# Kernel tuning notes

Hardware: AMD Instinct MI355X
Metric: run time of the kernel (lower is better)

The kernel has to match this reference:

```python
import jax, jax.numpy as jnp
import numpy as np

B, N, C = 4, 4096, 1024
H, D = 16, 64
EPS = 1e-6


def setup_inputs() -> dict:
    key = jax.random.key(0)
    ks = jax.random.split(key, 7)
    x = jax.random.normal(ks[0], (B, N, C), dtype=jnp.float32)
    # True = PAD (PyTorch convention)
    src_key_padding_mask = jax.random.randint(ks[1], (B, N), 0, 2).astype(jnp.bool_)
    s = 1.0 / np.sqrt(C)
    W_qkv = jax.random.uniform(ks[2], (3 * C, C), jnp.float32, -s, s)
    b_qkv = jax.random.uniform(ks[3], (3 * C,), jnp.float32, -s, s)
    W_out = jax.random.uniform(ks[4], (C, C), jnp.float32, -s, s)
    b_out = jax.random.uniform(ks[5], (C,), jnp.float32, -s, s)
    return {"x": x, "W_qkv": W_qkv, "b_qkv": b_qkv, "W_out": W_out,
            "b_out": b_out, "src_key_padding_mask": src_key_padding_mask}


def _phi(t):
    # elu(t) + 1  (alpha=1)
    return jnp.where(t > 0, t + 1.0, jnp.exp(t))


def reference(x, W_qkv, b_qkv, W_out, b_out, src_key_padding_mask):
    # qkv projection: [B,N,3C] -> [3,B,H,N,D]
    qkv = (x @ W_qkv.T + b_qkv).reshape(B, N, 3, H, D).transpose(2, 0, 3, 1, 4)
    q, k, v = qkv[0], qkv[1], qkv[2]
    qf = _phi(q)
    kf = _phi(k)
    valid = (~src_key_padding_mask).astype(kf.dtype)[:, None, :, None]  # [B,1,N,1]
    kf = kf * valid
    v = v * valid
    # kv state: [B,H,D,D]; z: [B,H,D]
    kv = jnp.einsum('bhnd,bhne->bhde', kf, v)
    z = kf.sum(axis=2)
    y_num = jnp.einsum('bhnd,bhde->bhne', qf, kv)      # [B,H,N,D]
    y_den = jnp.einsum('bhnd,bhd->bhn', qf, z)          # [B,H,N]
    y_den = jnp.maximum(y_den, EPS)[..., None]
    y = (y_num / y_den).transpose(0, 2, 1, 3).reshape(B, N, C)
    return y @ W_out.T + b_out
```

## Files before the change

kernel.cpp:

```cpp
#include <hip/hip_runtime.h>
#include <math.h>

#define B_ 4
#define N_ 4096
#define C_ 1024
#define H_ 16
#define D_ 64
#define M_ (B_*N_)
#define GK 1024
#define NCH 8
#define CHROWS (N_/NCH)

typedef __attribute__((ext_vector_type(8))) _Float16 f16x8;
typedef __attribute__((ext_vector_type(4))) _Float16 f16x4;
typedef __attribute__((ext_vector_type(4))) float f32x4;

__device__ __forceinline__ float phi_f(float t) {
  return (t > 0.0f) ? (t + 1.0f) : __expf(t);
}

#define GLOAD(gp, lp) __builtin_amdgcn_global_load_lds( \
    (const __attribute__((address_space(1))) unsigned int*)(gp), \
    (__attribute__((address_space(3))) unsigned int*)(lp), 16, 0, 0)

#define BARM() asm volatile("s_barrier" ::: "memory")
#define WAITV6() asm volatile("s_waitcnt vmcnt(6)" ::: "memory")
#define WAITV4() asm volatile("s_waitcnt vmcnt(4)" ::: "memory")
#define WAITV0() asm volatile("s_waitcnt vmcnt(0)" ::: "memory")
#define PRIO1() __builtin_amdgcn_s_setprio(1)
#define PRIO0() __builtin_amdgcn_s_setprio(0)

__device__ __forceinline__ f32x4 mfma16h(f16x8 a, f16x8 b, f32x4 c) {
  return __builtin_amdgcn_mfma_f32_16x16x32_f16(a, b, c, 0, 0, 0);
}

__global__ __launch_bounds__(256) void mask_detect_k(const unsigned int* __restrict__ w,
                                                     int* __restrict__ flag) {
  __shared__ int notint, notflt;
  if (threadIdx.x == 0) { notint = 0; notflt = 0; }
  __syncthreads();
  int ni = 0, nf = 0;
  for (int i = threadIdx.x; i < 4096; i += 256) {
    unsigned int v = w[i];
    if (v > 1u) ni = 1;
    if (v != 0u && v != 0x3F800000u) nf = 1;
  }
  if (ni) atomicOr(&notint, 1);
  if (nf) atomicOr(&notflt, 1);
  __syncthreads();
  if (threadIdx.x == 0) *flag = (!notint) ? 0 : ((!notflt) ? 1 : 2);
}

__global__ __launch_bounds__(256) void mask_convert_k(const void* __restrict__ mask,
                                                      const int* __restrict__ flag,
                                                      float* __restrict__ valid) {
  int i = blockIdx.x * 256 + threadIdx.x;
  int f = *flag;
  int m;
  if (f == 0)      m = ((const int*)mask)[i] != 0;
  else if (f == 1) m = ((const float*)mask)[i] != 0.0f;
  else             m = ((const unsigned char*)mask)[i] != 0;
  valid[i] = m ? 0.0f : 1.0f;
}

__global__ __launch_bounds__(256) void conv_f16_k(const float* __restrict__ src,
                                                  _Float16* __restrict__ dst, int n4) {
  int i = blockIdx.x * 256 + threadIdx.x;
  if (i >= n4) return;
  float4 v = ((const float4*)src)[i];
  f16x4 h;
  h[0] = (_Float16)v.x; h[1] = (_Float16)v.y;
  h[2] = (_Float16)v.z; h[3] = (_Float16)v.w;
  ((f16x4*)dst)[i] = h;
}

__global__ __launch_bounds__(256) void split_f16_k(const float* __restrict__ src,
                                                   _Float16* __restrict__ h,
                                                   _Float16* __restrict__ l, int n4) {
  int i = blockIdx.x * 256 + threadIdx.x;
  if (i >= n4) return;
  float4 v = ((const float4*)src)[i];
  f16x4 hv, lv;
  float vs[4] = {v.x, v.y, v.z, v.w};
#pragma unroll
  for (int q = 0; q < 4; ++q) {
    _Float16 hh = (_Float16)vs[q];
    _Float16 ll = (_Float16)(vs[q] - (float)hh);
    hv[q] = hh; lv[q] = ll;
  }
  ((f16x4*)h)[i] = hv;
  ((f16x4*)l)[i] = lv;
}


#define TILE_BODY(PC, DO_STAGE, DO_PRE, WAITK, KS)                             \
  {                                                                            \
    const _Float16* bb = lds + (PC) * 24576;                                   \
    const _Float16* nb = lds + (((PC) + 1) % 3) * 24576;                       \
    _Float16* sq = lds + (((PC) + 2) % 3) * 24576;                             \
    const size_t ks = (KS);                                                    \
                                     \
    _Pragma("unroll") for (int j = 0; j < 4; ++j)                              \
      bl[j] = *(const f16x8*)&bb[16384 + (wj * 4 + j) * 512 + lane * 8];       \
    if (DO_STAGE) { GLOAD(A + gA0 + ks, sq + w * 512);                         \
                    GLOAD(A + gA1 + ks, sq + 4096 + w * 512); }                \
    BARM();                                                                    \
    PRIO1();                                                                   \
    _Pragma("unroll") for (int i = 0; i < 4; ++i)                              \
      _Pragma("unroll") for (int j = 0; j < 4; ++j)                            \
        acc[i][j] = mfma16h(a0[i], bh[j], acc[i][j]);                          \
    PRIO0();                                                                   \
        \
    _Pragma("unroll") for (int i = 0; i < 4; ++i)                              \
      a1[i] = *(const f16x8*)&bb[(wm * 8 + 4 + i) * 512 + lane * 8];           \
    if (DO_STAGE) { GLOAD(Bh + gB0 + ks, sq + 8192 + w * 512);                 \
                    GLOAD(Bh + gB1 + ks, sq + 12288 + w * 512); }              \
    if ((WAITK) == 1) { WAITV4(); } else if ((WAITK) == 2) { WAITV0(); }       \
    BARM();                                                                    \
    PRIO1();                                                                   \
    _Pragma("unroll") for (int i = 0; i < 4; ++i)                              \
      _Pragma("unroll") for (int j = 0; j < 4; ++j)                            \
        acc[i][j] = mfma16h(a0[i], bl[j], acc[i][j]);                          \
    PRIO0();                                                                   \
                                \
    if (DO_PRE) { _Pragma("unroll") for (int i = 0; i < 4; ++i)                \
      a0[i] = *(const f16x8*)&nb[(wm * 8 + i) * 512 + lane * 8]; }             \
    if (DO_STAGE) { GLOAD(Bl + gB0 + ks, sq + 16384 + w * 512);                \
                    GLOAD(Bl + gB1 + ks, sq + 20480 + w * 512); }              \
    BARM();                                                                    \
    PRIO1();                                                                   \
    _Pragma("unroll") for (int i = 0; i < 4; ++i)                              \
      _Pragma("unroll") for (int j = 0; j < 4; ++j)                            \
        acc[4 + i][j] = mfma16h(a1[i], bh[j], acc[4 + i][j]);                  \
    PRIO0();                                                                   \
                                          \
    if (DO_PRE) { _Pragma("unroll") for (int j = 0; j < 4; ++j)                \
      bh[j] = *(const f16x8*)&nb[8192 + (wj * 4 + j) * 512 + lane * 8]; }      \
    BARM();                                                                    \
    PRIO1();                                                                   \
    _Pragma("unroll") for (int i = 0; i < 4; ++i)                              \
      _Pragma("unroll") for (int j = 0; j < 4; ++j)                            \
        acc[4 + i][j] = mfma16h(a1[i], bl[j], acc[4 + i][j]);                  \
    PRIO0();                                                                   \
  }

template <int EPI>
__global__ __launch_bounds__(512, 2) void gemm256_k(
    const _Float16* __restrict__ A,
    const _Float16* __restrict__ Bh, const _Float16* __restrict__ Bl,
    const float* __restrict__ bias, const float* __restrict__ valid,
    float* __restrict__ qf, float* __restrict__ kf, float* __restrict__ vv,
    float* __restrict__ outp, int jb, int jshift) {
  __shared__ _Float16 lds[73728];
  const int tid = threadIdx.x;
  const int lane = tid & 63, w = tid >> 6;
  const int lm = lane & 15, lq = lane >> 4;
  const int wm = w >> 2, wj = w & 3;

  const int nwg = gridDim.x;
  const int q8 = nwg >> 3;
  const int wid = (blockIdx.x & 7) * q8 + (blockIdx.x >> 3);
  const int j_blk = wid & ((1 << jshift) - 1);
  const int m_blk = wid >> jshift;
  const int m0 = m_blk * 256;
  const int jg0 = jb + j_blk * 256;

  const size_t gA0 = (size_t)(m0 + w * 16 + lm) * GK + lq * 8;
  const size_t gA1 = gA0 + (size_t)128 * GK;
  const size_t gB0 = (size_t)(jg0 + w * 16 + lm) * GK + lq * 8;
  const size_t gB1 = gB0 + (size_t)128 * GK;

#pragma unroll
  for (int tt = 0; tt < 2; ++tt) {
    _Float16* sq = lds + tt * 24576;
    const size_t ks = (size_t)tt * 32;
    GLOAD(A + gA0 + ks, sq + w * 512);
    GLOAD(A + gA1 + ks, sq + 4096 + w * 512);
    GLOAD(Bh + gB0 + ks, sq + 8192 + w * 512);
    GLOAD(Bh + gB1 + ks, sq + 12288 + w * 512);
    GLOAD(Bl + gB0 + ks, sq + 16384 + w * 512);
    GLOAD(Bl + gB1 + ks, sq + 20480 + w * 512);
  }
  WAITV6();
  BARM();

  f32x4 acc[8][4] = {};
  f16x8 a0[4], a1[4], bh[4], bl[4];
#pragma unroll
  for (int i = 0; i < 4; ++i)
    a0[i] = *(const f16x8*)&lds[(wm * 8 + i) * 512 + lane * 8];
#pragma unroll
  for (int j = 0; j < 4; ++j)
    bh[j] = *(const f16x8*)&lds[8192 + (wj * 4 + j) * 512 + lane * 8];

  for (int it = 0; it < 10; ++it) {
    const int t0 = 3 * it;
    TILE_BODY(0, true, true, 1, (size_t)(t0 + 2) * 32)
    TILE_BODY(1, true, true, 1, (size_t)(t0 + 3) * 32)
    TILE_BODY(2, true, true, 1, (size_t)(t0 + 4) * 32)
  }
  TILE_BODY(0, false, true, 2, 0)
  TILE_BODY(1, false, false, 0, 0)

  if (EPI == 0) {
    const int ty = jg0 >> 10;
    float* dst = (ty == 0) ? qf : ((ty == 1) ? kf : vv);
    float vld[8][4];
#pragma unroll
    for (int i = 0; i < 8; ++i)
#pragma unroll
      for (int r = 0; r < 4; ++r)
        vld[i][r] = (ty == 0) ? 1.0f : valid[m0 + wm * 128 + i * 16 + lq * 4 + r];
#pragma unroll
    for (int jt = 0; jt < 4; ++jt) {
      int jcol = jg0 + wj * 64 + jt * 16 + lm;
      float bj = bias[jcol];
      int c = jcol & 1023, hd = c >> 6, d = c & 63;
#pragma unroll
      for (int i = 0; i < 8; ++i)
#pragma unroll
        for (int r = 0; r < 4; ++r) {
          int m = m0 + wm * 128 + i * 16 + lq * 4 + r;
          int b = m >> 12, n = m & 4095;
          float val = acc[i][jt][r] + bj;
          if (ty <= 1) val = phi_f(val);
          if (ty >= 1) val *= vld[i][r];
          dst[(((size_t)(b * H_ + hd) * N_ + n) << 6) + d] = val;
        }
    }
  } else {
#pragma unroll
    for (int jt = 0; jt < 4; ++jt) {
      int jcol = jg0 + wj * 64 + jt * 16 + lm;
      float bj = bias[jcol];
#pragma unroll
      for (int i = 0; i < 8; ++i)
#pragma unroll
        for (int r = 0; r < 4; ++r) {
          int m = m0 + wm * 128 + i * 16 + lq * 4 + r;
          outp[(size_t)m * C_ + jcol] = acc[i][jt][r] + bj;
        }
    }
  }
}

__global__ __launch_bounds__(256) void kv_partial_k(
    const float* __restrict__ kf, const float* __restrict__ vv,
    float* __restrict__ kvp, float* __restrict__ zp) {
  const int bh = blockIdx.x, ch = blockIdx.y;
  const float* kfr = kf + ((size_t)bh * N_ + ch * CHROWS) * 64;
  const float* vr  = vv + ((size_t)bh * N_ + ch * CHROWS) * 64;
  __shared__ float ks[8][64], vs[8][64];
  const int tid = threadIdx.x;
  const int d0 = tid >> 2, eg = tid & 3;
  float acc[16] = {};
  float zacc = 0.f;
  for (int nb = 0; nb < CHROWS; nb += 8) {
    {
      int which = tid >> 7;
      int fl = tid & 127;
      int rr = fl >> 4, cc = (fl & 15) * 4;
      const float* src = which ? vr : kfr;
      float4 t4 = *(const float4*)&src[(size_t)(nb + rr) * 64 + cc];
      float* d = which ? &vs[rr][cc] : &ks[rr][cc];
      *(float4*)d = t4;
    }
    __syncthreads();
#pragma unroll
    for (int r = 0; r < 8; ++r) {
      float kd = ks[r][d0];
      if (eg == 0) zacc += kd;
#pragma unroll
      for (int i = 0; i < 16; ++i) acc[i] += kd * vs[r][eg * 16 + i];
    }
    __syncthreads();
  }
  size_t base = ((size_t)bh * NCH + ch) * 4096 + (size_t)d0 * 64 + eg * 16;
#pragma unroll
  for (int i = 0; i < 16; i += 4)
    *(float4*)&kvp[base + i] = make_float4(acc[i], acc[i+1], acc[i+2], acc[i+3]);
  if (eg == 0) zp[((size_t)bh * NCH + ch) * 64 + d0] = zacc;
}

__global__ __launch_bounds__(256) void kv_reduce_k(
    const float* __restrict__ kvp, const float* __restrict__ zp,
    float* __restrict__ kv, float* __restrict__ z) {
  const int bh = blockIdx.x, tid = threadIdx.x;
  for (int i = tid; i < 4096; i += 256) {
    float s = 0.f;
#pragma unroll
    for (int c = 0; c < NCH; ++c) s += kvp[((size_t)bh * NCH + c) * 4096 + i];
    kv[(size_t)bh * 4096 + i] = s;
  }
  if (tid < 64) {
    float s = 0.f;
#pragma unroll
    for (int c = 0; c < NCH; ++c) s += zp[((size_t)bh * NCH + c) * 64 + tid];
    z[bh * 64 + tid] = s;
  }
}

__global__ __launch_bounds__(256) void attn_apply_k(
    const float* __restrict__ qf, const float* __restrict__ kv,
    const float* __restrict__ z, _Float16* __restrict__ Y) {
  const int bh = blockIdx.x, nt = blockIdx.y;
  const int b = bh >> 4, hd = bh & 15;
  __shared__ float qs[128][65];
  __shared__ float kvs[64][68];
  __shared__ float zs[64];
  __shared__ float dens[128];
  const int tid = threadIdx.x;
  const float* qrow = qf + ((size_t)bh * N_ + nt * 128) * 64;
#pragma unroll
  for (int i = 0; i < 4; ++i) {
    int fl = tid + i * 256;
    int d = fl >> 4, cc = (fl & 15) * 4;
    float4 t4 = *(const float4*)&kv[(size_t)bh * 4096 + d * 64 + cc];
    kvs[d][cc] = t4.x; kvs[d][cc+1] = t4.y; kvs[d][cc+2] = t4.z; kvs[d][cc+3] = t4.w;
  }
  if (tid < 64) zs[tid] = z[bh * 64 + tid];
#pragma unroll
  for (int i = 0; i < 8; ++i) {
    int fl = tid + i * 256;
    int r = fl >> 4, cc = (fl & 15) * 4;
    float4 t4 = *(const float4*)&qrow[(size_t)r * 64 + cc];
    qs[r][cc] = t4.x; qs[r][cc+1] = t4.y; qs[r][cc+2] = t4.z; qs[r][cc+3] = t4.w;
  }
  __syncthreads();
  {
    int n = tid >> 1, half = tid & 1;
    float s = 0.f;
#pragma unroll
    for (int dd = 0; dd < 32; ++dd) {
      int d = half * 32 + dd;
      s += qs[n][d] * zs[d];
    }
    float other = __shfl_down(s, 1);
    if (half == 0) dens[n] = fmaxf(s + other, 1e-6f);
  }
  __syncthreads();
  const int ng = tid >> 3, eg = tid & 7;
  float acc[4][8] = {};
  for (int d = 0; d < 64; ++d) {
    float kvrow[8];
    *(float4*)&kvrow[0] = *(const float4*)&kvs[d][eg * 8];
    *(float4*)&kvrow[4] = *(const float4*)&kvs[d][eg * 8 + 4];
#pragma unroll
    for (int i = 0; i < 4; ++i) {
      float a = qs[ng * 4 + i][d];
#pragma unroll
      for (int j = 0; j < 8; ++j) acc[i][j] += a * kvrow[j];
    }
  }
#pragma unroll
  for (int i = 0; i < 4; ++i) {
    int nl = ng * 4 + i;
    int n = nt * 128 + nl;
    float inv = 1.0f / dens[nl];
    size_t off = ((size_t)b * N_ + n) * C_ + hd * 64 + eg * 8;
    f16x8 hv;
#pragma unroll
    for (int j = 0; j < 8; ++j) hv[j] = (_Float16)(acc[i][j] * inv);
    *(f16x8*)&Y[off] = hv;
  }
}

extern "C" void kernel_launch(void* const* d_in, const int* in_sizes, int n_in,
                              void* d_out, int out_size, void* d_ws, size_t ws_size,
                              hipStream_t stream) {
  const float* x      = (const float*)d_in[0];
  const float* W_qkv  = (const float*)d_in[1];
  const float* b_qkv  = (const float*)d_in[2];
  const float* W_out  = (const float*)d_in[3];
  const float* b_out  = (const float*)d_in[4];
  const void*  mask   = d_in[5];
  float* out = (float*)d_out;

  const size_t bhnd = (size_t)B_ * H_ * N_ * D_;
  float* ws = (float*)d_ws;
  float* buf1 = ws;
  float* buf2 = ws + bhnd;
  _Float16* Xh  = (_Float16*)(ws + 2 * bhnd);
  _Float16* Wqh = Xh + bhnd;
  _Float16* Wql = Wqh + (size_t)3072 * 1024;
  _Float16* Woh = Wql + (size_t)3072 * 1024;
  _Float16* Wol = Woh + (size_t)1024 * 1024;
  float* tail2 = (float*)(Wol + (size_t)1024 * 1024);
  float* kvp = tail2;
  float* zp  = kvp + (size_t)64 * NCH * 4096;
  float* kv  = zp + (size_t)64 * NCH * 64;
  float* z   = kv + (size_t)64 * 4096;
  float* valid = z + 64 * 64;
  int*   flag  = (int*)(valid + M_);

  _Float16* Y = (_Float16*)buf2;

  mask_detect_k<<<1, 256, 0, stream>>>((const unsigned int*)mask, flag);
  mask_convert_k<<<M_ / 256, 256, 0, stream>>>(mask, flag, valid);
  conv_f16_k<<<(int)(bhnd / 4 / 256), 256, 0, stream>>>(x, Xh, (int)(bhnd / 4));
  split_f16_k<<<3072 * 1024 / 4 / 256, 256, 0, stream>>>(W_qkv, Wqh, Wql, 3072 * 1024 / 4);
  split_f16_k<<<1024 * 1024 / 4 / 256, 256, 0, stream>>>(W_out, Woh, Wol, 1024 * 1024 / 4);
  gemm256_k<0><<<512, 512, 0, stream>>>(
      Xh, Wqh, Wql, b_qkv, valid, buf1, buf1, buf2, nullptr, 1024, 3);
  kv_partial_k<<<dim3(B_ * H_, NCH), 256, 0, stream>>>(buf1, buf2, kvp, zp);
  kv_reduce_k<<<B_ * H_, 256, 0, stream>>>(kvp, zp, kv, z);
  gemm256_k<0><<<256, 512, 0, stream>>>(
      Xh, Wqh, Wql, b_qkv, valid, buf1, buf1, buf2, nullptr, 0, 2);
  attn_apply_k<<<dim3(B_ * H_, N_ / 128), 256, 0, stream>>>(buf1, kv, z, Y);
  gemm256_k<1><<<256, 512, 0, stream>>>(
      Y, Woh, Wol, b_out, valid, nullptr, nullptr, nullptr, out, 0, 2);
}
```

Measured before the change: 493.8 us.

## Fuse prep kernels into one launch, reorder GEMM tile mapping, rework kv partial

Merges the mask detect/convert, x fp16 conversion and weight hi/lo split kernels into one prep kernel that dispatches on block index. Each mask block re-runs the 4096-word format check itself, which removes a launch and the flag buffer. The GEMM workgroup-to-tile mapping changes to m-fastest ordering (j_blk = wid>>6), which alters L2 reuse of weight versus activation tiles. kv_partial now uses 4x4 register tiles with k read straight from global memory and only v staged in LDS, instead of the 1x16 outer-product layout.

Result: faster. 483.8 us (-2.0%).

```diff
diff --git a/kernel.cpp b/kernel.cpp
--- a/kernel.cpp
+++ b/kernel.cpp
@@ -34,62 +34,67 @@
   return __builtin_amdgcn_mfma_f32_16x16x32_f16(a, b, c, 0, 0, 0);
 }
 
-__global__ __launch_bounds__(256) void mask_detect_k(const unsigned int* __restrict__ w,
-                                                     int* __restrict__ flag) {
-  __shared__ int notint, notflt;
-  if (threadIdx.x == 0) { notint = 0; notflt = 0; }
-  __syncthreads();
-  int ni = 0, nf = 0;
-  for (int i = threadIdx.x; i < 4096; i += 256) {
-    unsigned int v = w[i];
-    if (v > 1u) ni = 1;
-    if (v != 0u && v != 0x3F800000u) nf = 1;
-  }
-  if (ni) atomicOr(&notint, 1);
-  if (nf) atomicOr(&notflt, 1);
-  __syncthreads();
-  if (threadIdx.x == 0) *flag = (!notint) ? 0 : ((!notflt) ? 1 : 2);
-}
-
-__global__ __launch_bounds__(256) void mask_convert_k(const void* __restrict__ mask,
-                                                      const int* __restrict__ flag,
-                                                      float* __restrict__ valid) {
-  int i = blockIdx.x * 256 + threadIdx.x;
-  int f = *flag;
-  int m;
-  if (f == 0)      m = ((const int*)mask)[i] != 0;
-  else if (f == 1) m = ((const float*)mask)[i] != 0.0f;
-  else             m = ((const unsigned char*)mask)[i] != 0;
-  valid[i] = m ? 0.0f : 1.0f;
-}
-
-__global__ __launch_bounds__(256) void conv_f16_k(const float* __restrict__ src,
-                                                  _Float16* __restrict__ dst, int n4) {
-  int i = blockIdx.x * 256 + threadIdx.x;
-  if (i >= n4) return;
-  float4 v = ((const float4*)src)[i];
-  f16x4 h;
-  h[0] = (_Float16)v.x; h[1] = (_Float16)v.y;
-  h[2] = (_Float16)v.z; h[3] = (_Float16)v.w;
-  ((f16x4*)dst)[i] = h;
-}
-
-__global__ __launch_bounds__(256) void split_f16_k(const float* __restrict__ src,
-                                                   _Float16* __restrict__ h,
-                                                   _Float16* __restrict__ l, int n4) {
-  int i = blockIdx.x * 256 + threadIdx.x;
-  if (i >= n4) return;
-  float4 v = ((const float4*)src)[i];
-  f16x4 hv, lv;
-  float vs[4] = {v.x, v.y, v.z, v.w};
-#pragma unroll
-  for (int q = 0; q < 4; ++q) {
-    _Float16 hh = (_Float16)vs[q];
-    _Float16 ll = (_Float16)(vs[q] - (float)hh);
-    hv[q] = hh; lv[q] = ll;
-  }
-  ((f16x4*)h)[i] = hv;
-  ((f16x4*)l)[i] = lv;
+__global__ __launch_bounds__(256) void prep_k(
+    const float* __restrict__ x, _Float16* __restrict__ Xh,
+    const float* __restrict__ Wq, _Float16* __restrict__ Wqh, _Float16* __restrict__ Wql,
+    const float* __restrict__ Wo, _Float16* __restrict__ Woh, _Float16* __restrict__ Wol,
+    const void* __restrict__ mask, float* __restrict__ valid) {
+  const int b = blockIdx.x, tid = threadIdx.x;
+  if (b < 16384) {
+    int i = b * 256 + tid;
+    float4 v = ((const float4*)x)[i];
+    f16x4 h;
+    h[0] = (_Float16)v.x; h[1] = (_Float16)v.y;
+    h[2] = (_Float16)v.z; h[3] = (_Float16)v.w;
+    ((f16x4*)Xh)[i] = h;
+  } else if (b < 19456) {
+    int i = (b - 16384) * 256 + tid;
+    float4 v = ((const float4*)Wq)[i];
+    float vs[4] = {v.x, v.y, v.z, v.w};
+    f16x4 hv, lv;
+#pragma unroll
+    for (int q = 0; q < 4; ++q) {
+      _Float16 hh = (_Float16)vs[q];
+      lv[q] = (_Float16)(vs[q] - (float)hh);
+      hv[q] = hh;
+    }
+    ((f16x4*)Wqh)[i] = hv;
+    ((f16x4*)Wql)[i] = lv;
+  } else if (b < 20480) {
+    int i = (b - 19456) * 256 + tid;
+    float4 v = ((const float4*)Wo)[i];
+    float vs[4] = {v.x, v.y, v.z, v.w};
+    f16x4 hv, lv;
+#pragma unroll
+    for (int q = 0; q < 4; ++q) {
+      _Float16 hh = (_Float16)vs[q];
+      lv[q] = (_Float16)(vs[q] - (float)hh);
+      hv[q] = hh;
+    }
+    ((f16x4*)Woh)[i] = hv;
+    ((f16x4*)Wol)[i] = lv;
+  } else {
+    __shared__ unsigned int sni, snf;
+    if (tid == 0) { sni = 0u; snf = 0u; }
+    __syncthreads();
+    const unsigned int* mw = (const unsigned int*)mask;
+    unsigned int ni = 0, nf = 0;
+    for (int t = tid; t < 4096; t += 256) {
+      unsigned int v = mw[t];
+      ni |= (v > 1u) ? 1u : 0u;
+      nf |= (v != 0u && v != 0x3F800000u) ? 1u : 0u;
+    }
+    if (ni) atomicOr(&sni, 1u);
+    if (nf) atomicOr(&snf, 1u);
+    __syncthreads();
+    const int f = (!sni) ? 0 : ((!snf) ? 1 : 2);
+    int i = (b - 20480) * 256 + tid;
+    int m;
+    if (f == 0)      m = ((const int*)mask)[i] != 0;
+    else if (f == 1) m = ((const float*)mask)[i] != 0.0f;
+    else             m = ((const unsigned char*)mask)[i] != 0;
+    valid[i] = m ? 0.0f : 1.0f;
+  }
 }
 
 
@@ -150,7 +155,7 @@
     const _Float16* __restrict__ Bh, const _Float16* __restrict__ Bl,
     const float* __restrict__ bias, const float* __restrict__ valid,
     float* __restrict__ qf, float* __restrict__ kf, float* __restrict__ vv,
-    float* __restrict__ outp, int jb, int jshift) {
+    float* __restrict__ outp, int jb) {
   __shared__ _Float16 lds[73728];
   const int tid = threadIdx.x;
   const int lane = tid & 63, w = tid >> 6;
@@ -160,8 +165,8 @@
   const int nwg = gridDim.x;
   const int q8 = nwg >> 3;
   const int wid = (blockIdx.x & 7) * q8 + (blockIdx.x >> 3);
-  const int j_blk = wid & ((1 << jshift) - 1);
-  const int m_blk = wid >> jshift;
+  const int j_blk = wid >> 6;
+  const int m_blk = wid & 63;
   const int m0 = m_blk * 256;
   const int jg0 = jb + j_blk * 256;
 
@@ -250,36 +255,42 @@
   const int bh = blockIdx.x, ch = blockIdx.y;
   const float* kfr = kf + ((size_t)bh * N_ + ch * CHROWS) * 64;
   const float* vr  = vv + ((size_t)bh * N_ + ch * CHROWS) * 64;
-  __shared__ float ks[8][64], vs[8][64];
+  __shared__ float vs[16][64];
   const int tid = threadIdx.x;
-  const int d0 = tid >> 2, eg = tid & 3;
-  float acc[16] = {};
-  float zacc = 0.f;
-  for (int nb = 0; nb < CHROWS; nb += 8) {
-    {
-      int which = tid >> 7;
-      int fl = tid & 127;
-      int rr = fl >> 4, cc = (fl & 15) * 4;
-      const float* src = which ? vr : kfr;
-      float4 t4 = *(const float4*)&src[(size_t)(nb + rr) * 64 + cc];
-      float* d = which ? &vs[rr][cc] : &ks[rr][cc];
-      *(float4*)d = t4;
-    }
+  const int d4 = tid >> 4, e4 = tid & 15;
+  const int srow = tid >> 4, scol = (tid & 15) * 4;
+  float acc[4][4] = {};
+  float zacc[4] = {};
+  for (int nb = 0; nb < CHROWS; nb += 16) {
+    float4 st = *(const float4*)&vr[(size_t)(nb + srow) * 64 + scol];
     __syncthreads();
-#pragma unroll
-    for (int r = 0; r < 8; ++r) {
-      float kd = ks[r][d0];
-      if (eg == 0) zacc += kd;
-#pragma unroll
-      for (int i = 0; i < 16; ++i) acc[i] += kd * vs[r][eg * 16 + i];
-    }
+    *(float4*)&vs[srow][scol] = st;
+    float4 kq[16];
+#pragma unroll
+    for (int r = 0; r < 16; ++r)
+      kq[r] = *(const float4*)&kfr[(size_t)(nb + r) * 64 + d4 * 4];
     __syncthreads();
-  }
-  size_t base = ((size_t)bh * NCH + ch) * 4096 + (size_t)d0 * 64 + eg * 16;
-#pragma unroll
-  for (int i = 0; i < 16; i += 4)
-    *(float4*)&kvp[base + i] = make_float4(acc[i], acc[i+1], acc[i+2], acc[i+3]);
-  if (eg == 0) zp[((size_t)bh * NCH + ch) * 64 + d0] = zacc;
+#pragma unroll
+    for (int r = 0; r < 16; ++r) {
+      float4 vq = *(const float4*)&vs[r][e4 * 4];
+      float kk[4] = {kq[r].x, kq[r].y, kq[r].z, kq[r].w};
+      float vk[4] = {vq.x, vq.y, vq.z, vq.w};
+#pragma unroll
+      for (int di = 0; di < 4; ++di) {
+        if (e4 == 0) zacc[di] += kk[di];
+#pragma unroll
+        for (int ei = 0; ei < 4; ++ei) acc[di][ei] += kk[di] * vk[ei];
+      }
+    }
+  }
+  size_t base = ((size_t)bh * NCH + ch) * 4096 + (size_t)d4 * 4 * 64 + e4 * 4;
+#pragma unroll
+  for (int di = 0; di < 4; ++di)
+    *(float4*)&kvp[base + (size_t)di * 64] =
+        make_float4(acc[di][0], acc[di][1], acc[di][2], acc[di][3]);
+  if (e4 == 0)
+    *(float4*)&zp[((size_t)bh * NCH + ch) * 64 + d4 * 4] =
+        make_float4(zacc[0], zacc[1], zacc[2], zacc[3]);
 }
 
 __global__ __launch_bounds__(256) void kv_reduce_k(
@@ -391,22 +402,18 @@
   float* kv  = zp + (size_t)64 * NCH * 64;
   float* z   = kv + (size_t)64 * 4096;
   float* valid = z + 64 * 64;
-  int*   flag  = (int*)(valid + M_);
 
   _Float16* Y = (_Float16*)buf2;
 
-  mask_detect_k<<<1, 256, 0, stream>>>((const unsigned int*)mask, flag);
-  mask_convert_k<<<M_ / 256, 256, 0, stream>>>(mask, flag, valid);
-  conv_f16_k<<<(int)(bhnd / 4 / 256), 256, 0, stream>>>(x, Xh, (int)(bhnd / 4));
-  split_f16_k<<<3072 * 1024 / 4 / 256, 256, 0, stream>>>(W_qkv, Wqh, Wql, 3072 * 1024 / 4);
-  split_f16_k<<<1024 * 1024 / 4 / 256, 256, 0, stream>>>(W_out, Woh, Wol, 1024 * 1024 / 4);
+  prep_k<<<20544, 256, 0, stream>>>(x, Xh, W_qkv, Wqh, Wql, W_out, Woh, Wol,
+                                    mask, valid);
   gemm256_k<0><<<512, 512, 0, stream>>>(
-      Xh, Wqh, Wql, b_qkv, valid, buf1, buf1, buf2, nullptr, 1024, 3);
+      Xh, Wqh, Wql, b_qkv, valid, buf1, buf1, buf2, nullptr, 1024);
   kv_partial_k<<<dim3(B_ * H_, NCH), 256, 0, stream>>>(buf1, buf2, kvp, zp);
   kv_reduce_k<<<B_ * H_, 256, 0, stream>>>(kvp, zp, kv, z);
   gemm256_k<0><<<256, 512, 0, stream>>>(
-      Xh, Wqh, Wql, b_qkv, valid, buf1, buf1, buf2, nullptr, 0, 2);
+      Xh, Wqh, Wql, b_qkv, valid, buf1, buf1, buf2, nullptr, 0);
   attn_apply_k<<<dim3(B_ * H_, N_ / 128), 256, 0, stream>>>(buf1, kv, z, Y);
   gemm256_k<1><<<256, 512, 0, stream>>>(
-      Y, Woh, Wol, b_out, valid, nullptr, nullptr, nullptr, out, 0, 2);
-}
+      Y, Woh, Wol, b_out, valid, nullptr, nullptr, nullptr, out, 0);
+}
```
